# Kernel optimization log

Measured on AMD Instinct MI355X. Metric: run time of the kernel, lower is better.

The kernel has to match this reference:

```python
import jax, jax.numpy as jnp
import numpy as np

RC = 6.0            # cosine cutoff radius (Angstrom)
N_ANGULAR = 128     # module init arg; output dim = 3*N_ANGULAR
EPS = 1e-12


def cosine_cutoff(d):
    # Behler-style cosine cutoff: 0.5*(cos(pi*d/rc)+1) for d < rc, else 0
    return jnp.where(d < RC, 0.5 * (jnp.cos(jnp.pi * d / RC) + 1.0), 0.0)


def setup_inputs() -> dict:
    key = jax.random.key(0)
    k1, k2, k3, k4 = jax.random.split(key, 4)
    B, N, M = 8, 4096, 96
    L = 20.0  # box length
    positions = jax.random.uniform(k1, (B, N, 3), dtype=jnp.float32) * L
    cell = jnp.tile(jnp.eye(3, dtype=jnp.float32) * L, (B, 1, 1))
    neighbors = jax.random.randint(k2, (B, N, M), 0, N, dtype=jnp.int32)
    offsets = jax.random.randint(k3, (B, N, M, 3), -1, 2).astype(jnp.float32)
    mask = (jax.random.uniform(k4, (B, N, M)) > 0.1).astype(jnp.float32)
    return {"positions": positions, "cell": cell, "offsets": offsets,
            "mask": mask, "neighbors": neighbors}


def reference(positions, cell, offsets, mask, neighbors):
    B, N, M = neighbors.shape
    # gather neighbor positions: pos_j[b,n,m,:] = positions[b, neighbors[b,n,m], :]
    idx = neighbors.reshape(B, N * M)
    pos_j = jnp.take_along_axis(positions, idx[:, :, None], axis=1).reshape(B, N, M, 3)
    # displacement vectors with periodic offsets (offsets in cell coordinates)
    dis_vec = pos_j - positions[:, :, None, :] + jnp.einsum('bnmi,bij->bnmj', offsets, cell)
    distances = jnp.sqrt(jnp.sum(dis_vec * dis_vec, axis=-1) + EPS)  # [B,N,M]
    # cutoff / distance, zeroed where mask == 0
    cut = jnp.where(mask != 0.0, cosine_cutoff(distances) / distances, 0.0)
    # sort neighbors by descending cut value, gather cut-weighted vectors in that order
    order = jnp.argsort(-cut, axis=-1)                       # [B,N,M]
    cut_vec = cut[..., None] * dis_vec                       # [B,N,M,3]
    cut_vec = jnp.take_along_axis(cut_vec, order[..., None], axis=2)
    cut_vec = cut_vec.reshape(B, N, M * 3)
    # scatter into zero-padded descriptor of width 3*n_angular
    f = jnp.zeros((B, N, N_ANGULAR * 3), dtype=positions.dtype)
    f = f.at[:, :, : M * 3].set(cut_vec)
    return f
```

## Files before the change

### kernel.cpp

```cpp
#include <hip/hip_runtime.h>
#include <math.h>

#define M_NB   96
#define OUT_W  384
#define NATOM  4096
#define WPB    16
#define LOWM   0x00000000FFFFFFFFull
#define HIGHM  0xFFFFFFFF00000000ull

__device__ __forceinline__ void merge3(float4& a4, float2& a2, int base,
                                       float v0, float v1, float v2, int lane)
{
    const int f4lo = 4 * lane;
    const int f2lo = 256 + 2 * lane;
    const float v[3] = {v0, v1, v2};
    #pragma unroll
    for (int t = 0; t < 3; ++t) {
        const int idx = base + t;
        if      (idx == f4lo)     a4.x = v[t];
        else if (idx == f4lo + 1) a4.y = v[t];
        else if (idx == f4lo + 2) a4.z = v[t];
        else if (idx == f4lo + 3) a4.w = v[t];
        else if (idx == f2lo)     a2.x = v[t];
        else if (idx == f2lo + 1) a2.y = v[t];
    }
}

__global__ __launch_bounds__(64 * WPB, 8) void deepmd_angular_kernel(
    const float* __restrict__ positions,
    const float* __restrict__ cell,
    const float* __restrict__ offsets,
    const float* __restrict__ mask,
    const int*   __restrict__ neighbors,
    float*       __restrict__ out,
    int N)
{
    __shared__ float4 pos4_s[NATOM];

    const int tid  = threadIdx.x;
    const int wv   = tid >> 6;
    const int lane = tid & 63;

    const int p0 = blockIdx.x * (WPB * 4);
    const int b  = p0 / N;

    {
        const float* pb_ = positions + (size_t)b * N * 3;
        for (int a = tid; a < NATOM; a += 64 * WPB) {
            const float3 v = *(const float3*)(pb_ + 3 * a);
            pos4_s[a] = make_float4(v.x, v.y, v.z, 0.f);
        }
    }
    __syncthreads();

    const float* cb = cell + (size_t)b * 9;
    const float c00 = cb[0], c01 = cb[1], c02 = cb[2];
    const float c10 = cb[3], c11 = cb[4], c12 = cb[5];
    const float c20 = cb[6], c21 = cb[7], c22 = cb[8];

    #pragma unroll
    for (int it = 0; it < 2; ++it) {
        const int q0   = p0 + wv * 4 + it * 2;
        const long base = (long)q0 * M_NB;
        const long e0 = base + lane, e1 = e0 + 64, e2 = e0 + 128;

        const int   j0 = neighbors[e0], j1 = neighbors[e1], j2 = neighbors[e2];
        const float m0 = mask[e0],      m1 = mask[e1],      m2 = mask[e2];
        const float3 o0 = *(const float3*)(offsets + e0 * 3);
        const float3 o1 = *(const float3*)(offsets + e1 * 3);
        const float3 o2 = *(const float3*)(offsets + e2 * 3);

        const int nn0 = q0 - b * N;
        const float4 pi0 = pos4_s[nn0];
        const float4 pi1 = pos4_s[nn0 + 1];
        const float4 pj0 = pos4_s[j0];
        const float4 pj1 = pos4_s[j1];
        const float4 pj2 = pos4_s[j2];
        const float4 pa  = (lane < 32) ? pi0 : pi1;

        float w0x = pj0.x - pi0.x + o0.x * c00 + o0.y * c10 + o0.z * c20;
        float w0y = pj0.y - pi0.y + o0.x * c01 + o0.y * c11 + o0.z * c21;
        float w0z = pj0.z - pi0.z + o0.x * c02 + o0.y * c12 + o0.z * c22;
        float d   = sqrtf(w0x * w0x + w0y * w0y + w0z * w0z + 1e-12f);
        float c0v = 0.f;
        if (m0 != 0.f && d < 6.f)
            c0v = 0.5f * (__cosf(d * 0.52359877559829887f) + 1.f) / d;
        w0x *= c0v; w0y *= c0v; w0z *= c0v;

        float w1x = pj1.x - pa.x + o1.x * c00 + o1.y * c10 + o1.z * c20;
        float w1y = pj1.y - pa.y + o1.x * c01 + o1.y * c11 + o1.z * c21;
        float w1z = pj1.z - pa.z + o1.x * c02 + o1.y * c12 + o1.z * c22;
        d = sqrtf(w1x * w1x + w1y * w1y + w1z * w1z + 1e-12f);
        float c1v = 0.f;
        if (m1 != 0.f && d < 6.f)
            c1v = 0.5f * (__cosf(d * 0.52359877559829887f) + 1.f) / d;
        w1x *= c1v; w1y *= c1v; w1z *= c1v;

        float w2x = pj2.x - pi1.x + o2.x * c00 + o2.y * c10 + o2.z * c20;
        float w2y = pj2.y - pi1.y + o2.x * c01 + o2.y * c11 + o2.z * c21;
        float w2z = pj2.z - pi1.z + o2.x * c02 + o2.y * c12 + o2.z * c22;
        d = sqrtf(w2x * w2x + w2y * w2y + w2z * w2z + 1e-12f);
        float c2v = 0.f;
        if (m2 != 0.f && d < 6.f)
            c2v = 0.5f * (__cosf(d * 0.52359877559829887f) + 1.f) / d;
        w2x *= c2v; w2y *= c2v; w2z *= c2v;

        float4 a4 = make_float4(0.f, 0.f, 0.f, 0.f);
        float2 a2 = make_float2(0.f, 0.f);
        unsigned long long t = __ballot(c0v != 0.f);
        while (t) {
            const int s = (int)__builtin_ctzll(t); t &= t - 1;
            const float c = __shfl(c0v, s);
            const int rank = __popcll(__ballot(c0v > c))
                           + __popcll(__ballot(c1v > c) & LOWM)
                           + __popcll(__ballot(c0v == c) & ((1ull << s) - 1ull));
            merge3(a4, a2, 3 * rank,
                   __shfl(w0x, s), __shfl(w0y, s), __shfl(w0z, s), lane);
        }
        t = __ballot(c1v != 0.f) & LOWM;
        while (t) {
            const int s = (int)__builtin_ctzll(t); t &= t - 1;
            const float c = __shfl(c1v, s);
            const int rank = __popcll(__ballot(c0v > c))
                           + __popcll(__ballot(c1v > c) & LOWM)
                           + __popcll(__ballot(c0v == c))
                           + __popcll(__ballot(c1v == c) & LOWM & ((1ull << s) - 1ull));
            merge3(a4, a2, 3 * rank,
                   __shfl(w1x, s), __shfl(w1y, s), __shfl(w1z, s), lane);
        }
        float* row0 = out + (size_t)q0 * OUT_W;
        ((float4*)row0)[lane] = a4;
        ((float2*)(row0 + 256))[lane] = a2;

        float4 b4 = make_float4(0.f, 0.f, 0.f, 0.f);
        float2 b2 = make_float2(0.f, 0.f);
        t = __ballot(c1v != 0.f) & HIGHM;
        while (t) {
            const int s = (int)__builtin_ctzll(t); t &= t - 1;
            const float c = __shfl(c1v, s);
            const int rank = __popcll(__ballot(c1v > c) & HIGHM)
                           + __popcll(__ballot(c2v > c))
                           + __popcll(__ballot(c1v == c) & HIGHM & ((1ull << s) - 1ull));
            merge3(b4, b2, 3 * rank,
                   __shfl(w1x, s), __shfl(w1y, s), __shfl(w1z, s), lane);
        }
        t = __ballot(c2v != 0.f);
        while (t) {
            const int s = (int)__builtin_ctzll(t); t &= t - 1;
            const float c = __shfl(c2v, s);
            const int rank = __popcll(__ballot(c1v > c) & HIGHM)
                           + __popcll(__ballot(c2v > c))
                           + __popcll(__ballot(c1v == c) & HIGHM)
                           + __popcll(__ballot(c2v == c) & ((1ull << s) - 1ull));
            merge3(b4, b2, 3 * rank,
                   __shfl(w2x, s), __shfl(w2y, s), __shfl(w2z, s), lane);
        }
        float* row1 = out + (size_t)(q0 + 1) * OUT_W;
        ((float4*)row1)[lane] = b4;
        ((float2*)(row1 + 256))[lane] = b2;
    }
}

extern "C" void kernel_launch(void* const* d_in, const int* in_sizes, int n_in,
                              void* d_out, int out_size, void* d_ws, size_t ws_size,
                              hipStream_t stream) {
    const float* positions = (const float*)d_in[0];
    const float* cell      = (const float*)d_in[1];
    const float* offsets   = (const float*)d_in[2];
    const float* mask      = (const float*)d_in[3];
    const int*   neighbors = (const int*)d_in[4];
    float*       out       = (float*)d_out;

    const int BN = in_sizes[0] / 3;
    const int B  = in_sizes[1] / 9;
    const int N  = BN / B;

    dim3 block(64 * WPB, 1, 1);
    dim3 grid(BN / (WPB * 4), 1, 1);
    deepmd_angular_kernel<<<grid, block, 0, stream>>>(
        positions, cell, offsets, mask, neighbors, out, N);
}
```

Measured before the change: 116.4 us.

## Prefetch next pair's neighbor data in registers and halve block size

```diff
diff --git a/kernel.cpp b/kernel.cpp
--- a/kernel.cpp
+++ b/kernel.cpp
@@ -4,7 +4,8 @@
 #define M_NB   96
 #define OUT_W  384
 #define NATOM  4096
-#define WPB    16
+#define WPB    8
+#define ITERS  4
 #define LOWM   0x00000000FFFFFFFFull
 #define HIGHM  0xFFFFFFFF00000000ull
 
@@ -26,7 +27,7 @@
     }
 }
 
-__global__ __launch_bounds__(64 * WPB, 8) void deepmd_angular_kernel(
+__global__ __launch_bounds__(64 * WPB, 4) void deepmd_angular_kernel(
     const float* __restrict__ positions,
     const float* __restrict__ cell,
     const float* __restrict__ offsets,
@@ -41,7 +42,7 @@
     const int wv   = tid >> 6;
     const int lane = tid & 63;
 
-    const int p0 = blockIdx.x * (WPB * 4);
+    const int p0 = blockIdx.x * (WPB * 2 * ITERS);
     const int b  = p0 / N;
 
     {
@@ -58,47 +59,68 @@
     const float c10 = cb[3], c11 = cb[4], c12 = cb[5];
     const float c20 = cb[6], c21 = cb[7], c22 = cb[8];
 
+    const int  r0    = p0 + wv * (2 * ITERS);
+    const long base0 = (long)r0 * M_NB;
+
+    int    pj0, pj1, pj2;
+    float  pm0, pm1, pm2;
+    float3 po0, po1, po2;
+    {
+        const long e0 = base0 + lane, e1 = e0 + 64, e2 = e0 + 128;
+        pj0 = neighbors[e0]; pj1 = neighbors[e1]; pj2 = neighbors[e2];
+        pm0 = mask[e0];      pm1 = mask[e1];      pm2 = mask[e2];
+        po0 = *(const float3*)(offsets + e0 * 3);
+        po1 = *(const float3*)(offsets + e1 * 3);
+        po2 = *(const float3*)(offsets + e2 * 3);
+    }
+
     #pragma unroll
-    for (int it = 0; it < 2; ++it) {
-        const int q0   = p0 + wv * 4 + it * 2;
-        const long base = (long)q0 * M_NB;
-        const long e0 = base + lane, e1 = e0 + 64, e2 = e0 + 128;
-
-        const int   j0 = neighbors[e0], j1 = neighbors[e1], j2 = neighbors[e2];
-        const float m0 = mask[e0],      m1 = mask[e1],      m2 = mask[e2];
-        const float3 o0 = *(const float3*)(offsets + e0 * 3);
-        const float3 o1 = *(const float3*)(offsets + e1 * 3);
-        const float3 o2 = *(const float3*)(offsets + e2 * 3);
+    for (int it = 0; it < ITERS; ++it) {
+        const int q0 = r0 + it * 2;
+
+        const int    j0 = pj0, j1 = pj1, j2 = pj2;
+        const float  m0 = pm0, m1 = pm1, m2 = pm2;
+        const float3 o0 = po0, o1 = po1, o2 = po2;
+
+        if (it + 1 < ITERS) {
+            const long e0 = base0 + (long)(it + 1) * 192 + lane;
+            const long e1 = e0 + 64, e2 = e0 + 128;
+            pj0 = neighbors[e0]; pj1 = neighbors[e1]; pj2 = neighbors[e2];
+            pm0 = mask[e0];      pm1 = mask[e1];      pm2 = mask[e2];
+            po0 = *(const float3*)(offsets + e0 * 3);
+            po1 = *(const float3*)(offsets + e1 * 3);
+            po2 = *(const float3*)(offsets + e2 * 3);
+        }
 
         const int nn0 = q0 - b * N;
         const float4 pi0 = pos4_s[nn0];
         const float4 pi1 = pos4_s[nn0 + 1];
-        const float4 pj0 = pos4_s[j0];
-        const float4 pj1 = pos4_s[j1];
-        const float4 pj2 = pos4_s[j2];
+        const float4 pj0v = pos4_s[j0];
+        const float4 pj1v = pos4_s[j1];
+        const float4 pj2v = pos4_s[j2];
         const float4 pa  = (lane < 32) ? pi0 : pi1;
 
-        float w0x = pj0.x - pi0.x + o0.x * c00 + o0.y * c10 + o0.z * c20;
-        float w0y = pj0.y - pi0.y + o0.x * c01 + o0.y * c11 + o0.z * c21;
-        float w0z = pj0.z - pi0.z + o0.x * c02 + o0.y * c12 + o0.z * c22;
+        float w0x = pj0v.x - pi0.x + o0.x * c00 + o0.y * c10 + o0.z * c20;
+        float w0y = pj0v.y - pi0.y + o0.x * c01 + o0.y * c11 + o0.z * c21;
+        float w0z = pj0v.z - pi0.z + o0.x * c02 + o0.y * c12 + o0.z * c22;
         float d   = sqrtf(w0x * w0x + w0y * w0y + w0z * w0z + 1e-12f);
         float c0v = 0.f;
         if (m0 != 0.f && d < 6.f)
             c0v = 0.5f * (__cosf(d * 0.52359877559829887f) + 1.f) / d;
         w0x *= c0v; w0y *= c0v; w0z *= c0v;
 
-        float w1x = pj1.x - pa.x + o1.x * c00 + o1.y * c10 + o1.z * c20;
-        float w1y = pj1.y - pa.y + o1.x * c01 + o1.y * c11 + o1.z * c21;
-        float w1z = pj1.z - pa.z + o1.x * c02 + o1.y * c12 + o1.z * c22;
+        float w1x = pj1v.x - pa.x + o1.x * c00 + o1.y * c10 + o1.z * c20;
+        float w1y = pj1v.y - pa.y + o1.x * c01 + o1.y * c11 + o1.z * c21;
+        float w1z = pj1v.z - pa.z + o1.x * c02 + o1.y * c12 + o1.z * c22;
         d = sqrtf(w1x * w1x + w1y * w1y + w1z * w1z + 1e-12f);
         float c1v = 0.f;
         if (m1 != 0.f && d < 6.f)
             c1v = 0.5f * (__cosf(d * 0.52359877559829887f) + 1.f) / d;
         w1x *= c1v; w1y *= c1v; w1z *= c1v;
 
-        float w2x = pj2.x - pi1.x + o2.x * c00 + o2.y * c10 + o2.z * c20;
-        float w2y = pj2.y - pi1.y + o2.x * c01 + o2.y * c11 + o2.z * c21;
-        float w2z = pj2.z - pi1.z + o2.x * c02 + o2.y * c12 + o2.z * c22;
+        float w2x = pj2v.x - pi1.x + o2.x * c00 + o2.y * c10 + o2.z * c20;
+        float w2y = pj2v.y - pi1.y + o2.x * c01 + o2.y * c11 + o2.z * c21;
+        float w2z = pj2v.z - pi1.z + o2.x * c02 + o2.y * c12 + o2.z * c22;
         d = sqrtf(w2x * w2x + w2y * w2y + w2z * w2z + 1e-12f);
         float c2v = 0.f;
         if (m2 != 0.f && d < 6.f)
@@ -176,7 +198,7 @@
     const int N  = BN / B;
 
     dim3 block(64 * WPB, 1, 1);
-    dim3 grid(BN / (WPB * 4), 1, 1);
+    dim3 grid(BN / (WPB * 2 * ITERS), 1, 1);
     deepmd_angular_kernel<<<grid, block, 0, stream>>>(
         positions, cell, offsets, mask, neighbors, out, N);
 }
```

Result: no change. 116.4 us (+0.0%).

## Double-buffer per-row inputs into LDS with async global_load_lds pipeline

Applied to the files above, without the earlier changes.

```diff
diff --git a/kernel.cpp b/kernel.cpp
--- a/kernel.cpp
+++ b/kernel.cpp
@@ -4,9 +4,52 @@
 #define M_NB   96
 #define OUT_W  384
 #define NATOM  4096
-#define WPB    16
+#define WAVES  4
+#define NTHR   256
+#define RPP    8
+#define PHASES 8
+#define PHASE_FLOATS 3840
+#define POS_FLOATS   12288
+#define POS_CHUNKS   48
+#define PH_CHUNKS    15
+#define OFFS_CH      9
+#define NBR_CH       3
+#define LDS_FLOATS   (POS_FLOATS + 2 * PHASE_FLOATS)
 #define LOWM   0x00000000FFFFFFFFull
 #define HIGHM  0xFFFFFFFF00000000ull
+
+#define MEMBAR() asm volatile("" ::: "memory")
+#define VMW(n)   asm volatile("s_waitcnt vmcnt(" #n ")" ::: "memory")
+
+__device__ __forceinline__ void sbar() {
+    MEMBAR(); __builtin_amdgcn_s_barrier(); MEMBAR();
+}
+
+__device__ __forceinline__ void gll16(const void* g, void* l) {
+    __builtin_amdgcn_global_load_lds(
+        (const __attribute__((address_space(1))) void*)g,
+        (__attribute__((address_space(3))) void*)l, 16, 0, 0);
+}
+
+__device__ __forceinline__ void stage8(const float* __restrict__ offsets,
+                                       const int* __restrict__ neighbors,
+                                       const float* __restrict__ mask,
+                                       int firstRow, float* dst, int wv, int lane)
+{
+    const size_t r = (size_t)firstRow;
+    const float4* o4 = (const float4*)offsets  + r * 72;
+    const int4*   n4 = (const int4*)neighbors + r * 24;
+    const float4* m4 = (const float4*)mask     + r * 24;
+    for (int i = wv; i < PH_CHUNKS; i += WAVES) {
+        float* d = dst + i * 256;
+        if (i < OFFS_CH)
+            gll16(o4 + (size_t)i * 64 + lane, d);
+        else if (i < OFFS_CH + NBR_CH)
+            gll16(n4 + (size_t)(i - OFFS_CH) * 64 + lane, d);
+        else
+            gll16(m4 + (size_t)(i - OFFS_CH - NBR_CH) * 64 + lane, d);
+    }
+}
 
 __device__ __forceinline__ void merge3(float4& a4, float2& a2, int base,
                                        float v0, float v1, float v2, int lane)
@@ -26,7 +69,7 @@
     }
 }
 
-__global__ __launch_bounds__(64 * WPB, 8) void deepmd_angular_kernel(
+__global__ __launch_bounds__(NTHR, 2) void deepmd_angular_kernel(
     const float* __restrict__ positions,
     const float* __restrict__ cell,
     const float* __restrict__ offsets,
@@ -35,48 +78,56 @@
     float*       __restrict__ out,
     int N)
 {
-    __shared__ float4 pos4_s[NATOM];
+    extern __shared__ float lds[];
+    float* posT = lds;
+    float* bufA = lds + POS_FLOATS;
+    float* bufB = bufA + PHASE_FLOATS;
 
     const int tid  = threadIdx.x;
     const int wv   = tid >> 6;
     const int lane = tid & 63;
 
-    const int p0 = blockIdx.x * (WPB * 4);
-    const int b  = p0 / N;
-
-    {
-        const float* pb_ = positions + (size_t)b * N * 3;
-        for (int a = tid; a < NATOM; a += 64 * WPB) {
-            const float3 v = *(const float3*)(pb_ + 3 * a);
-            pos4_s[a] = make_float4(v.x, v.y, v.z, 0.f);
-        }
-    }
-    __syncthreads();
+    const int row0 = blockIdx.x * (RPP * PHASES);
+    const int b    = row0 / N;
 
     const float* cb = cell + (size_t)b * 9;
     const float c00 = cb[0], c01 = cb[1], c02 = cb[2];
     const float c10 = cb[3], c11 = cb[4], c12 = cb[5];
     const float c20 = cb[6], c21 = cb[7], c22 = cb[8];
 
+    {
+        const float4* p4 = (const float4*)(positions + (size_t)b * N * 3);
+        for (int i = wv; i < POS_CHUNKS; i += WAVES)
+            gll16(p4 + (size_t)i * 64 + lane, posT + i * 256);
+    }
+    stage8(offsets, neighbors, mask, row0,       bufA, wv, lane);
+    stage8(offsets, neighbors, mask, row0 + RPP, bufB, wv, lane);
+
+    if (wv < 3) { VMW(4); } else { VMW(3); }
+    __builtin_amdgcn_sched_barrier(0);
+    sbar();
+
     #pragma unroll
-    for (int it = 0; it < 2; ++it) {
-        const int q0   = p0 + wv * 4 + it * 2;
-        const long base = (long)q0 * M_NB;
-        const long e0 = base + lane, e1 = e0 + 64, e2 = e0 + 128;
-
-        const int   j0 = neighbors[e0], j1 = neighbors[e1], j2 = neighbors[e2];
-        const float m0 = mask[e0],      m1 = mask[e1],      m2 = mask[e2];
-        const float3 o0 = *(const float3*)(offsets + e0 * 3);
-        const float3 o1 = *(const float3*)(offsets + e1 * 3);
-        const float3 o2 = *(const float3*)(offsets + e2 * 3);
+    for (int p = 0; p < PHASES; ++p) {
+        float* buf = (p & 1) ? bufB : bufA;
+
+        const int q0 = row0 + p * RPP + wv * 2;
+        const int e0 = wv * 192 + lane, e1 = e0 + 64, e2 = e0 + 128;
+        const int*   nbrp = (const int*)(buf + OFFS_CH * 256);
+        const float* mskp = buf + (OFFS_CH + NBR_CH) * 256;
+        const int   j0 = nbrp[e0], j1 = nbrp[e1], j2 = nbrp[e2];
+        const float m0 = mskp[e0], m1 = mskp[e1], m2 = mskp[e2];
+        const float3 o0 = *(const float3*)(buf + 3 * e0);
+        const float3 o1 = *(const float3*)(buf + 3 * e1);
+        const float3 o2 = *(const float3*)(buf + 3 * e2);
 
         const int nn0 = q0 - b * N;
-        const float4 pi0 = pos4_s[nn0];
-        const float4 pi1 = pos4_s[nn0 + 1];
-        const float4 pj0 = pos4_s[j0];
-        const float4 pj1 = pos4_s[j1];
-        const float4 pj2 = pos4_s[j2];
-        const float4 pa  = (lane < 32) ? pi0 : pi1;
+        const float3 pi0 = *(const float3*)(posT + 3 * nn0);
+        const float3 pi1 = *(const float3*)(posT + 3 * (nn0 + 1));
+        const float3 pj0 = *(const float3*)(posT + 3 * j0);
+        const float3 pj1 = *(const float3*)(posT + 3 * j1);
+        const float3 pj2 = *(const float3*)(posT + 3 * j2);
+        const float3 pa  = (lane < 32) ? pi0 : pi1;
 
         float w0x = pj0.x - pi0.x + o0.x * c00 + o0.y * c10 + o0.z * c20;
         float w0y = pj0.y - pi0.y + o0.x * c01 + o0.y * c11 + o0.z * c21;
@@ -128,9 +179,9 @@
             merge3(a4, a2, 3 * rank,
                    __shfl(w1x, s), __shfl(w1y, s), __shfl(w1z, s), lane);
         }
-        float* row0 = out + (size_t)q0 * OUT_W;
-        ((float4*)row0)[lane] = a4;
-        ((float2*)(row0 + 256))[lane] = a2;
+        float* row0p = out + (size_t)q0 * OUT_W;
+        ((float4*)row0p)[lane] = a4;
+        ((float2*)(row0p + 256))[lane] = a2;
 
         float4 b4 = make_float4(0.f, 0.f, 0.f, 0.f);
         float2 b2 = make_float2(0.f, 0.f);
@@ -155,9 +206,23 @@
             merge3(b4, b2, 3 * rank,
                    __shfl(w2x, s), __shfl(w2y, s), __shfl(w2z, s), lane);
         }
-        float* row1 = out + (size_t)(q0 + 1) * OUT_W;
-        ((float4*)row1)[lane] = b4;
-        ((float2*)(row1 + 256))[lane] = b2;
+        float* row1p = out + (size_t)(q0 + 1) * OUT_W;
+        ((float4*)row1p)[lane] = b4;
+        ((float2*)(row1p + 256))[lane] = b2;
+
+        if (p + 2 < PHASES) {
+            sbar();
+            stage8(offsets, neighbors, mask, row0 + (p + 2) * RPP, buf, wv, lane);
+        }
+        if (p + 1 < PHASES) {
+            if (p + 2 < PHASES) {
+                if (wv < 3) { VMW(8); } else { VMW(7); }
+            } else {
+                VMW(4);
+            }
+            __builtin_amdgcn_sched_barrier(0);
+            sbar();
+        }
     }
 }
 
@@ -175,8 +240,16 @@
     const int B  = in_sizes[1] / 9;
     const int N  = BN / B;
 
-    dim3 block(64 * WPB, 1, 1);
-    dim3 grid(BN / (WPB * 4), 1, 1);
-    deepmd_angular_kernel<<<grid, block, 0, stream>>>(
+    static bool attr_set = false;
+    if (!attr_set) {
+        hipFuncSetAttribute(reinterpret_cast<const void*>(deepmd_angular_kernel),
+                            hipFuncAttributeMaxDynamicSharedMemorySize,
+                            LDS_FLOATS * 4);
+        attr_set = true;
+    }
+
+    dim3 block(NTHR, 1, 1);
+    dim3 grid(BN / (RPP * PHASES), 1, 1);
+    deepmd_angular_kernel<<<grid, block, LDS_FLOATS * 4, stream>>>(
         positions, cell, offsets, mask, neighbors, out, N);
 }
```

Result: slower. 123.0 us (+5.7%).

## Drop shared-memory position staging and software-pipeline per-wave neighbor loads

Applied to the files above, without the earlier changes.

```diff
diff --git a/kernel.cpp b/kernel.cpp
--- a/kernel.cpp
+++ b/kernel.cpp
@@ -3,10 +3,30 @@
 
 #define M_NB   96
 #define OUT_W  384
-#define NATOM  4096
-#define WPB    16
+#define WAVES  8
+#define PAIRS_PW 8
 #define LOWM   0x00000000FFFFFFFFull
 #define HIGHM  0xFFFFFFFF00000000ull
+
+struct Pref {
+    int    j0, j1, j2;
+    float  m0, m1, m2;
+    float3 o0, o1, o2;
+};
+
+__device__ __forceinline__ void ldpref(Pref& P,
+                                       const int* __restrict__ neighbors,
+                                       const float* __restrict__ mask,
+                                       const float* __restrict__ offsets,
+                                       long e0)
+{
+    const long e1 = e0 + 64, e2 = e0 + 128;
+    P.j0 = neighbors[e0]; P.j1 = neighbors[e1]; P.j2 = neighbors[e2];
+    P.m0 = mask[e0];      P.m1 = mask[e1];      P.m2 = mask[e2];
+    P.o0 = *(const float3*)(offsets + e0 * 3);
+    P.o1 = *(const float3*)(offsets + e1 * 3);
+    P.o2 = *(const float3*)(offsets + e2 * 3);
+}
 
 __device__ __forceinline__ void merge3(float4& a4, float2& a2, int base,
                                        float v0, float v1, float v2, int lane)
@@ -26,7 +46,103 @@
     }
 }
 
-__global__ __launch_bounds__(64 * WPB, 8) void deepmd_angular_kernel(
+__device__ __forceinline__ void consume_pair(
+    const Pref& P, int q0, int nbase,
+    const float* __restrict__ posg, float* __restrict__ out,
+    float c00, float c01, float c02, float c10, float c11, float c12,
+    float c20, float c21, float c22, int lane)
+{
+    const int nn0 = q0 - nbase;
+    const float3 pi0 = *(const float3*)(posg + 3 * nn0);
+    const float3 pi1 = *(const float3*)(posg + 3 * (nn0 + 1));
+    const float3 pj0 = *(const float3*)(posg + 3 * P.j0);
+    const float3 pj1 = *(const float3*)(posg + 3 * P.j1);
+    const float3 pj2 = *(const float3*)(posg + 3 * P.j2);
+    const float3 pa  = (lane < 32) ? pi0 : pi1;
+
+    float w0x = pj0.x - pi0.x + P.o0.x * c00 + P.o0.y * c10 + P.o0.z * c20;
+    float w0y = pj0.y - pi0.y + P.o0.x * c01 + P.o0.y * c11 + P.o0.z * c21;
+    float w0z = pj0.z - pi0.z + P.o0.x * c02 + P.o0.y * c12 + P.o0.z * c22;
+    float d   = sqrtf(w0x * w0x + w0y * w0y + w0z * w0z + 1e-12f);
+    float c0v = 0.f;
+    if (P.m0 != 0.f && d < 6.f)
+        c0v = 0.5f * (__cosf(d * 0.52359877559829887f) + 1.f) / d;
+    w0x *= c0v; w0y *= c0v; w0z *= c0v;
+
+    float w1x = pj1.x - pa.x + P.o1.x * c00 + P.o1.y * c10 + P.o1.z * c20;
+    float w1y = pj1.y - pa.y + P.o1.x * c01 + P.o1.y * c11 + P.o1.z * c21;
+    float w1z = pj1.z - pa.z + P.o1.x * c02 + P.o1.y * c12 + P.o1.z * c22;
+    d = sqrtf(w1x * w1x + w1y * w1y + w1z * w1z + 1e-12f);
+    float c1v = 0.f;
+    if (P.m1 != 0.f && d < 6.f)
+        c1v = 0.5f * (__cosf(d * 0.52359877559829887f) + 1.f) / d;
+    w1x *= c1v; w1y *= c1v; w1z *= c1v;
+
+    float w2x = pj2.x - pi1.x + P.o2.x * c00 + P.o2.y * c10 + P.o2.z * c20;
+    float w2y = pj2.y - pi1.y + P.o2.x * c01 + P.o2.y * c11 + P.o2.z * c21;
+    float w2z = pj2.z - pi1.z + P.o2.x * c02 + P.o2.y * c12 + P.o2.z * c22;
+    d = sqrtf(w2x * w2x + w2y * w2y + w2z * w2z + 1e-12f);
+    float c2v = 0.f;
+    if (P.m2 != 0.f && d < 6.f)
+        c2v = 0.5f * (__cosf(d * 0.52359877559829887f) + 1.f) / d;
+    w2x *= c2v; w2y *= c2v; w2z *= c2v;
+
+    float4 a4 = make_float4(0.f, 0.f, 0.f, 0.f);
+    float2 a2 = make_float2(0.f, 0.f);
+    unsigned long long t = __ballot(c0v != 0.f);
+    while (t) {
+        const int s = (int)__builtin_ctzll(t); t &= t - 1;
+        const float c = __shfl(c0v, s);
+        const int rank = __popcll(__ballot(c0v > c))
+                       + __popcll(__ballot(c1v > c) & LOWM)
+                       + __popcll(__ballot(c0v == c) & ((1ull << s) - 1ull));
+        merge3(a4, a2, 3 * rank,
+               __shfl(w0x, s), __shfl(w0y, s), __shfl(w0z, s), lane);
+    }
+    t = __ballot(c1v != 0.f) & LOWM;
+    while (t) {
+        const int s = (int)__builtin_ctzll(t); t &= t - 1;
+        const float c = __shfl(c1v, s);
+        const int rank = __popcll(__ballot(c0v > c))
+                       + __popcll(__ballot(c1v > c) & LOWM)
+                       + __popcll(__ballot(c0v == c))
+                       + __popcll(__ballot(c1v == c) & LOWM & ((1ull << s) - 1ull));
+        merge3(a4, a2, 3 * rank,
+               __shfl(w1x, s), __shfl(w1y, s), __shfl(w1z, s), lane);
+    }
+    float* row0 = out + (size_t)q0 * OUT_W;
+    ((float4*)row0)[lane] = a4;
+    ((float2*)(row0 + 256))[lane] = a2;
+
+    float4 b4 = make_float4(0.f, 0.f, 0.f, 0.f);
+    float2 b2 = make_float2(0.f, 0.f);
+    t = __ballot(c1v != 0.f) & HIGHM;
+    while (t) {
+        const int s = (int)__builtin_ctzll(t); t &= t - 1;
+        const float c = __shfl(c1v, s);
+        const int rank = __popcll(__ballot(c1v > c) & HIGHM)
+                       + __popcll(__ballot(c2v > c))
+                       + __popcll(__ballot(c1v == c) & HIGHM & ((1ull << s) - 1ull));
+        merge3(b4, b2, 3 * rank,
+               __shfl(w1x, s), __shfl(w1y, s), __shfl(w1z, s), lane);
+    }
+    t = __ballot(c2v != 0.f);
+    while (t) {
+        const int s = (int)__builtin_ctzll(t); t &= t - 1;
+        const float c = __shfl(c2v, s);
+        const int rank = __popcll(__ballot(c1v > c) & HIGHM)
+                       + __popcll(__ballot(c2v > c))
+                       + __popcll(__ballot(c1v == c) & HIGHM)
+                       + __popcll(__ballot(c2v == c) & ((1ull << s) - 1ull));
+        merge3(b4, b2, 3 * rank,
+               __shfl(w2x, s), __shfl(w2y, s), __shfl(w2z, s), lane);
+    }
+    float* row1 = out + (size_t)(q0 + 1) * OUT_W;
+    ((float4*)row1)[lane] = b4;
+    ((float2*)(row1 + 256))[lane] = b2;
+}
+
+__global__ __launch_bounds__(64 * WAVES, 4) void deepmd_angular_kernel(
     const float* __restrict__ positions,
     const float* __restrict__ cell,
     const float* __restrict__ offsets,
@@ -35,129 +151,38 @@
     float*       __restrict__ out,
     int N)
 {
-    __shared__ float4 pos4_s[NATOM];
-
     const int tid  = threadIdx.x;
     const int wv   = tid >> 6;
     const int lane = tid & 63;
 
-    const int p0 = blockIdx.x * (WPB * 4);
-    const int b  = p0 / N;
-
-    {
-        const float* pb_ = positions + (size_t)b * N * 3;
-        for (int a = tid; a < NATOM; a += 64 * WPB) {
-            const float3 v = *(const float3*)(pb_ + 3 * a);
-            pos4_s[a] = make_float4(v.x, v.y, v.z, 0.f);
-        }
-    }
-    __syncthreads();
+    const int rows_pb = WAVES * PAIRS_PW * 2;
+    const int row0    = blockIdx.x * rows_pb;
+    const int b       = row0 / N;
+    const int nbase   = b * N;
+
+    const float* posg = positions + (size_t)b * N * 3;
 
     const float* cb = cell + (size_t)b * 9;
     const float c00 = cb[0], c01 = cb[1], c02 = cb[2];
     const float c10 = cb[3], c11 = cb[4], c12 = cb[5];
     const float c20 = cb[6], c21 = cb[7], c22 = cb[8];
 
+    const int  wrow  = row0 + wv * (PAIRS_PW * 2);
+    const long wbase = (long)wrow * M_NB;
+
+    Pref PA, PB, PC;
+    ldpref(PA, neighbors, mask, offsets, wbase + 0L * 192 + lane);
+    ldpref(PB, neighbors, mask, offsets, wbase + 1L * 192 + lane);
+    ldpref(PC, neighbors, mask, offsets, wbase + 2L * 192 + lane);
+
     #pragma unroll
-    for (int it = 0; it < 2; ++it) {
-        const int q0   = p0 + wv * 4 + it * 2;
-        const long base = (long)q0 * M_NB;
-        const long e0 = base + lane, e1 = e0 + 64, e2 = e0 + 128;
-
-        const int   j0 = neighbors[e0], j1 = neighbors[e1], j2 = neighbors[e2];
-        const float m0 = mask[e0],      m1 = mask[e1],      m2 = mask[e2];
-        const float3 o0 = *(const float3*)(offsets + e0 * 3);
-        const float3 o1 = *(const float3*)(offsets + e1 * 3);
-        const float3 o2 = *(const float3*)(offsets + e2 * 3);
-
-        const int nn0 = q0 - b * N;
-        const float4 pi0 = pos4_s[nn0];
-        const float4 pi1 = pos4_s[nn0 + 1];
-        const float4 pj0 = pos4_s[j0];
-        const float4 pj1 = pos4_s[j1];
-        const float4 pj2 = pos4_s[j2];
-        const float4 pa  = (lane < 32) ? pi0 : pi1;
-
-        float w0x = pj0.x - pi0.x + o0.x * c00 + o0.y * c10 + o0.z * c20;
-        float w0y = pj0.y - pi0.y + o0.x * c01 + o0.y * c11 + o0.z * c21;
-        float w0z = pj0.z - pi0.z + o0.x * c02 + o0.y * c12 + o0.z * c22;
-        float d   = sqrtf(w0x * w0x + w0y * w0y + w0z * w0z + 1e-12f);
-        float c0v = 0.f;
-        if (m0 != 0.f && d < 6.f)
-            c0v = 0.5f * (__cosf(d * 0.52359877559829887f) + 1.f) / d;
-        w0x *= c0v; w0y *= c0v; w0z *= c0v;
-
-        float w1x = pj1.x - pa.x + o1.x * c00 + o1.y * c10 + o1.z * c20;
-        float w1y = pj1.y - pa.y + o1.x * c01 + o1.y * c11 + o1.z * c21;
-        float w1z = pj1.z - pa.z + o1.x * c02 + o1.y * c12 + o1.z * c22;
-        d = sqrtf(w1x * w1x + w1y * w1y + w1z * w1z + 1e-12f);
-        float c1v = 0.f;
-        if (m1 != 0.f && d < 6.f)
-            c1v = 0.5f * (__cosf(d * 0.52359877559829887f) + 1.f) / d;
-        w1x *= c1v; w1y *= c1v; w1z *= c1v;
-
-        float w2x = pj2.x - pi1.x + o2.x * c00 + o2.y * c10 + o2.z * c20;
-        float w2y = pj2.y - pi1.y + o2.x * c01 + o2.y * c11 + o2.z * c21;
-        float w2z = pj2.z - pi1.z + o2.x * c02 + o2.y * c12 + o2.z * c22;
-        d = sqrtf(w2x * w2x + w2y * w2y + w2z * w2z + 1e-12f);
-        float c2v = 0.f;
-        if (m2 != 0.f && d < 6.f)
-            c2v = 0.5f * (__cosf(d * 0.52359877559829887f) + 1.f) / d;
-        w2x *= c2v; w2y *= c2v; w2z *= c2v;
-
-        float4 a4 = make_float4(0.f, 0.f, 0.f, 0.f);
-        float2 a2 = make_float2(0.f, 0.f);
-        unsigned long long t = __ballot(c0v != 0.f);
-        while (t) {
-            const int s = (int)__builtin_ctzll(t); t &= t - 1;
-            const float c = __shfl(c0v, s);
-            const int rank = __popcll(__ballot(c0v > c))
-                           + __popcll(__ballot(c1v > c) & LOWM)
-                           + __popcll(__ballot(c0v == c) & ((1ull << s) - 1ull));
-            merge3(a4, a2, 3 * rank,
-                   __shfl(w0x, s), __shfl(w0y, s), __shfl(w0z, s), lane);
-        }
-        t = __ballot(c1v != 0.f) & LOWM;
-        while (t) {
-            const int s = (int)__builtin_ctzll(t); t &= t - 1;
-            const float c = __shfl(c1v, s);
-            const int rank = __popcll(__ballot(c0v > c))
-                           + __popcll(__ballot(c1v > c) & LOWM)
-                           + __popcll(__ballot(c0v == c))
-                           + __popcll(__ballot(c1v == c) & LOWM & ((1ull << s) - 1ull));
-            merge3(a4, a2, 3 * rank,
-                   __shfl(w1x, s), __shfl(w1y, s), __shfl(w1z, s), lane);
-        }
-        float* row0 = out + (size_t)q0 * OUT_W;
-        ((float4*)row0)[lane] = a4;
-        ((float2*)(row0 + 256))[lane] = a2;
-
-        float4 b4 = make_float4(0.f, 0.f, 0.f, 0.f);
-        float2 b2 = make_float2(0.f, 0.f);
-        t = __ballot(c1v != 0.f) & HIGHM;
-        while (t) {
-            const int s = (int)__builtin_ctzll(t); t &= t - 1;
-            const float c = __shfl(c1v, s);
-            const int rank = __popcll(__ballot(c1v > c) & HIGHM)
-                           + __popcll(__ballot(c2v > c))
-                           + __popcll(__ballot(c1v == c) & HIGHM & ((1ull << s) - 1ull));
-            merge3(b4, b2, 3 * rank,
-                   __shfl(w1x, s), __shfl(w1y, s), __shfl(w1z, s), lane);
-        }
-        t = __ballot(c2v != 0.f);
-        while (t) {
-            const int s = (int)__builtin_ctzll(t); t &= t - 1;
-            const float c = __shfl(c2v, s);
-            const int rank = __popcll(__ballot(c1v > c) & HIGHM)
-                           + __popcll(__ballot(c2v > c))
-                           + __popcll(__ballot(c1v == c) & HIGHM)
-                           + __popcll(__ballot(c2v == c) & ((1ull << s) - 1ull));
-            merge3(b4, b2, 3 * rank,
-                   __shfl(w2x, s), __shfl(w2y, s), __shfl(w2z, s), lane);
-        }
-        float* row1 = out + (size_t)(q0 + 1) * OUT_W;
-        ((float4*)row1)[lane] = b4;
-        ((float2*)(row1 + 256))[lane] = b2;
+    for (int k = 0; k < PAIRS_PW; ++k) {
+        Pref& cur = (k % 3 == 0) ? PA : ((k % 3 == 1) ? PB : PC);
+        consume_pair(cur, wrow + 2 * k, nbase, posg, out,
+                     c00, c01, c02, c10, c11, c12, c20, c21, c22, lane);
+        if (k + 3 < PAIRS_PW)
+            ldpref(cur, neighbors, mask, offsets,
+                   wbase + (long)(k + 3) * 192 + lane);
     }
 }
 
@@ -175,8 +200,9 @@
     const int B  = in_sizes[1] / 9;
     const int N  = BN / B;
 
-    dim3 block(64 * WPB, 1, 1);
-    dim3 grid(BN / (WPB * 4), 1, 1);
+    const int rows_pb = WAVES * PAIRS_PW * 2;
+    dim3 block(64 * WAVES, 1, 1);
+    dim3 grid(BN / rows_pb, 1, 1);
     deepmd_angular_kernel<<<grid, block, 0, stream>>>(
         positions, cell, offsets, mask, neighbors, out, N);
 }
```

Result: slower. 134.1 us (+15.2%).
